# Performance work log

Hardware: AMD Instinct MI355X
Metric: run time of the kernel (lower is better)

## Reference

```python
import jax, jax.numpy as jnp
import numpy as np

B, C, H, D, W = 1, 32, 32, 32, 32   # batch, channels, 3D grid
M1 = M2 = M3 = 16                   # fourier modes kept per dim
KS = 3                              # spatial attention kernel size
MEM = 5                             # memory slots
EPS = 1e-5
N = H * D * W


def _gelu(x):
    return jax.nn.gelu(x, approximate=False)  # torch exact GELU


def _gn(x):
    # GroupNorm(1, C) without affine: normalize over (C,H,D,W) per sample
    mu = jnp.mean(x, axis=(1, 2, 3, 4), keepdims=True)
    var = jnp.var(x, axis=(1, 2, 3, 4), keepdims=True)
    return (x - mu) * jax.lax.rsqrt(var + EPS)


def _spectral_conv(x, wr, wi):
    # classic 3D FNO spectral conv: keep low modes (4 corner blocks in dims H,D; low block in rfft dim W)
    xf = jnp.fft.rfftn(x, axes=(2, 3, 4))                 # (B,C,H,D,W//2+1) complex64
    w = wr + 1j * wi                                      # (4,Cin,Cout,M1,M2,M3)
    of = jnp.zeros((x.shape[0], C, H, D, W // 2 + 1), xf.dtype)
    corners = [(slice(0, M1), slice(0, M2)), (slice(H - M1, H), slice(0, M2)),
               (slice(0, M1), slice(D - M2, D)), (slice(H - M1, H), slice(D - M2, D))]
    for i, (s1, s2) in enumerate(corners):
        of = of.at[:, :, s1, s2, :M3].set(
            jnp.einsum('bixyz,ioxyz->boxyz', xf[:, :, s1, s2, :M3], w[i]))
    return jnp.fft.irfftn(of, s=(H, D, W), axes=(2, 3, 4))


def _forward(x, t, prev_memory, w_spec_r, w_spec_i, norm1_g, norm1_b,
             mlp_w1, mlp_b1, mlp_w2, mlp_b2, tin_gw, tin_gb, tin_bw, tin_bb,
             q_w, q_b, k_w, k_b, v_w, v_b, mem_key, mem_value,
             gate_w, gate_b, gru_wih, gru_whh, gru_bih, gru_bhh):
    skip1 = x
    skip2 = _gelu(x)
    # spectral conv -> GroupNorm(affine) + residual -> gelu
    h = _spectral_conv(x, w_spec_r, w_spec_i)
    h = _gelu(_gn(h) * norm1_g[None, :, None, None, None]
              + norm1_b[None, :, None, None, None] + skip1)
    # pointwise Conv1d MLP over channels
    hf = h.reshape(B, C, N)
    u = _gelu(jnp.einsum('oc,bcn->bon', mlp_w1, hf) + mlp_b1[None, :, None])
    hf = jnp.einsum('oc,bcn->bon', mlp_w2, u) + mlp_b2[None, :, None]
    h = hf.reshape(B, C, H, D, W)
    # time-conditioned instance norm: gamma/beta from 1x1 conv over t (B,C)
    gamma = (jnp.einsum('oc,bc->bo', tin_gw, t) + tin_gb)[:, :, None, None, None]
    beta = (jnp.einsum('oc,bc->bo', tin_bw, t) + tin_bb)[:, :, None, None, None]
    h = gamma * _gn(h) + beta
    # ---- spatial attention with memory ----
    pad = KS // 2
    xp = jnp.pad(h, ((0, 0), (0, 0), (pad, pad), (pad, pad), (pad, pad)))
    # 3D unfold: (B,C,27,N) patches via 27 shifted views
    patches = jnp.stack([xp[:, :, i:i + H, j:j + D, l:l + W]
                         for i in range(KS) for j in range(KS) for l in range(KS)],
                        axis=2).reshape(B, C, KS ** 3, N)
    hf = h.reshape(B, C, N)
    q = jnp.einsum('oc,bcn->bon', q_w, hf) + q_b[None, :, None]              # (B,C,N)
    k_sp = jnp.einsum('oc,bcmn->bomn', k_w, patches) + k_b[None, :, None, None]
    v_sp = jnp.einsum('oc,bcmn->bomn', v_w, patches) + v_b[None, :, None, None]
    mem_k = jnp.broadcast_to(mem_key[None, :, :, None], (B, C, MEM, N))
    mem_v = jnp.broadcast_to(mem_value[None, :, :, None], (B, C, MEM, N))
    k = jnp.concatenate([mem_k, k_sp], axis=2)                               # (B,C,32,N)
    v = jnp.concatenate([mem_v, v_sp], axis=2)
    attn = jax.nn.softmax(q[:, :, None, :] * k / jnp.sqrt(jnp.float32(C)), axis=2)
    out = jnp.sum(attn * v, axis=2)                                          # (B,C,N)
    cat = jnp.concatenate([hf, out], axis=1)                                 # (B,2C,N)
    gate = jax.nn.sigmoid(jnp.einsum('oc,bcn->bon', gate_w, cat) + gate_b[None, :, None])
    out = gate * out + (1.0 - gate) * hf
    out = out.reshape(B, C, H, D, W)
    # GRUCell memory update from spatially pooled features
    m_in = jnp.mean(out, axis=(2, 3, 4))                                     # (B,C)
    gi = m_in @ gru_wih.T + gru_bih
    gh = prev_memory @ gru_whh.T + gru_bhh
    ir, iz, inn = jnp.split(gi, 3, axis=1)
    hr, hz, hn = jnp.split(gh, 3, axis=1)
    r = jax.nn.sigmoid(ir + hr)
    z = jax.nn.sigmoid(iz + hz)
    n = jnp.tanh(inn + r * hn)
    new_memory = (1.0 - z) * n + z * prev_memory                             # (B,C)
    return out + skip2, new_memory


def setup_inputs():
    key = jax.random.key(0)
    ks = jax.random.split(key, 20)
    def rn(k, shape, s):
        return jax.random.normal(k, shape, jnp.float32) * s
    spec_scale = 1.0 / (C * C)
    return dict(
        x=jax.random.normal(ks[0], (B, C, H, D, W), jnp.float32),
        t=jax.random.normal(ks[1], (B, C), jnp.float32),
        prev_memory=jnp.zeros((B, C), jnp.float32),
        w_spec_r=rn(ks[2], (4, C, C, M1, M2, M3), spec_scale),
        w_spec_i=rn(ks[3], (4, C, C, M1, M2, M3), spec_scale),
        norm1_g=jnp.ones((C,), jnp.float32),
        norm1_b=jnp.zeros((C,), jnp.float32),
        mlp_w1=rn(ks[4], (C // 2, C), 0.1), mlp_b1=jnp.zeros((C // 2,), jnp.float32),
        mlp_w2=rn(ks[5], (C, C // 2), 0.1), mlp_b2=jnp.zeros((C,), jnp.float32),
        tin_gw=rn(ks[6], (C, C), 0.1), tin_gb=jnp.ones((C,), jnp.float32),
        tin_bw=rn(ks[7], (C, C), 0.1), tin_bb=jnp.zeros((C,), jnp.float32),
        q_w=rn(ks[8], (C, C), 0.1), q_b=jnp.zeros((C,), jnp.float32),
        k_w=rn(ks[9], (C, C), 0.1), k_b=jnp.zeros((C,), jnp.float32),
        v_w=rn(ks[10], (C, C), 0.1), v_b=jnp.zeros((C,), jnp.float32),
        mem_key=jax.random.normal(ks[11], (C, MEM), jnp.float32),
        mem_value=jax.random.normal(ks[12], (C, MEM), jnp.float32),
        gate_w=rn(ks[13], (C, 2 * C), 0.1), gate_b=jnp.zeros((C,), jnp.float32),
        gru_wih=rn(ks[14], (3 * C, C), 0.1), gru_whh=rn(ks[15], (3 * C, C), 0.1),
        gru_bih=jnp.zeros((3 * C,), jnp.float32), gru_bhh=jnp.zeros((3 * C,), jnp.float32),
    )


def reference(x, t, prev_memory, w_spec_r, w_spec_i, norm1_g, norm1_b,
              mlp_w1, mlp_b1, mlp_w2, mlp_b2, tin_gw, tin_gb, tin_bw, tin_bb,
              q_w, q_b, k_w, k_b, v_w, v_b, mem_key, mem_value,
              gate_w, gate_b, gru_wih, gru_whh, gru_bih, gru_bhh):
    return _forward(x, t, prev_memory, w_spec_r, w_spec_i, norm1_g, norm1_b,
                    mlp_w1, mlp_b1, mlp_w2, mlp_b2, tin_gw, tin_gb, tin_bw, tin_bb,
                    q_w, q_b, k_w, k_b, v_w, v_b, mem_key, mem_value,
                    gate_w, gate_b, gru_wih, gru_whh, gru_bih, gru_bhh)
```

## Files before the change

### kernel.cpp

```cpp
#include <hip/hip_runtime.h>
#include <hip/hip_bf16.h>
#include <math.h>

#define NSP 32768
#define NZ 17

__device__ __forceinline__ float geluf(float x){
    return 0.5f * x * (1.0f + erff(x * 0.70710678118654752f));
}
__device__ __forceinline__ float sigmoidf_(float x){
    return 1.0f / (1.0f + expf(-x));
}


__global__ void k_rfft_w(const float* __restrict__ x, float* __restrict__ Ar, float* __restrict__ Ai){
    __shared__ float tile[32*33];
    __shared__ float ct[32], st[32];
    int b = blockIdx.x;
    int t = threadIdx.x;
    if (t < 32){ float ang = 6.283185307179586477f * (float)t / 32.0f; ct[t] = cosf(ang); st[t] = sinf(ang); }
    const float* src = x + b * 1024;
    for (int j = t; j < 1024; j += 256) tile[(j & 31) * 33 + (j >> 5)] = src[j];
    __syncthreads();
    for (int idx = t; idx < 544; idx += 256){
        int d = idx / 17, z = idx - d * 17;
        float sr = 0.f, si = 0.f;
        #pragma unroll
        for (int w = 0; w < 32; ++w){
            int a = (z * w) & 31;
            float v = tile[w * 33 + d];
            sr += v * ct[a];
            si -= v * st[a];
        }
        int o = (b * 32 + d) * NZ + z;
        Ar[o] = sr; Ai[o] = si;
    }
}

__global__ void k_fft_d(const float* __restrict__ Ar, const float* __restrict__ Ai,
                        float* __restrict__ Br, float* __restrict__ Bi){
    __shared__ float ir[544], ii[544];
    __shared__ float ct[32], st[32];
    int b = blockIdx.x, t = threadIdx.x;
    if (t < 32){ float ang = 6.283185307179586477f * (float)t / 32.0f; ct[t] = cosf(ang); st[t] = sinf(ang); }
    const float* pr = Ar + b * 544;
    const float* pi = Ai + b * 544;
    for (int j = t; j < 544; j += 256){ ir[j] = pr[j]; ii[j] = pi[j]; }
    __syncthreads();
    for (int idx = t; idx < 544; idx += 256){
        int kd = idx / 17, z = idx - kd * 17;
        float sr = 0.f, si = 0.f;
        #pragma unroll
        for (int d = 0; d < 32; ++d){
            int a = (kd * d) & 31;
            float c = ct[a], s = st[a];
            float vr = ir[d * 17 + z], vi = ii[d * 17 + z];
            sr += vr * c + vi * s;
            si += vi * c - vr * s;
        }
        Br[b * 544 + idx] = sr; Bi[b * 544 + idx] = si;
    }
}

__global__ void k_fft_h(const float* __restrict__ Br, const float* __restrict__ Bi,
                        float* __restrict__ Ar, float* __restrict__ Ai){
    __shared__ float ir[544], ii[544];
    __shared__ float ct[32], st[32];
    int b = blockIdx.x, t = threadIdx.x;
    int c = b >> 5, d = b & 31;
    if (t < 32){ float ang = 6.283185307179586477f * (float)t / 32.0f; ct[t] = cosf(ang); st[t] = sinf(ang); }
    for (int j = t; j < 544; j += 256){
        int h = j / 17, z = j - h * 17;
        int g = ((c * 32 + h) * 32 + d) * NZ + z;
        ir[j] = Br[g]; ii[j] = Bi[g];
    }
    __syncthreads();
    for (int idx = t; idx < 544; idx += 256){
        int kh = idx / 17, z = idx - kh * 17;
        float sr = 0.f, si = 0.f;
        #pragma unroll
        for (int h = 0; h < 32; ++h){
            int a = (kh * h) & 31;
            float c2 = ct[a], s2 = st[a];
            float vr = ir[h * 17 + z], vi = ii[h * 17 + z];
            sr += vr * c2 + vi * s2;
            si += vi * c2 - vr * s2;
        }
        int g = ((c * 32 + kh) * 32 + d) * NZ + z;
        Ar[g] = sr; Ai[g] = si;
    }
}

__global__ void k_modemul(const float* __restrict__ Xr, const float* __restrict__ Xi,
                          const float* __restrict__ Wr, const float* __restrict__ Wi,
                          float* __restrict__ Or, float* __restrict__ Oi){
    __shared__ float xr[32 * 64], xi[32 * 64];
    int b = blockIdx.x;
    int corner = b >> 6;
    int xm = (b >> 2) & 15;
    int ymg = b & 3;
    int xg = xm + ((corner & 1) << 4);
    int ybase = ymg * 4 + ((corner >> 1) << 4);
    int t = threadIdx.x;
    for (int idx = t; idx < 2048; idx += 256){
        int i = idx >> 6, m = idx & 63;
        int y = ybase + (m >> 4), z = m & 15;
        int g = ((i * 32 + xg) * 32 + y) * NZ + z;
        xr[idx] = Xr[g]; xi[idx] = Xi[g];
    }
    if (t < 128){
        int o = t >> 2, y = ybase + (t & 3);
        int g = ((o * 32 + xg) * 32 + y) * NZ + 16;
        Or[g] = 0.f; Oi[g] = 0.f;
    }
    __syncthreads();
    int wv = t >> 6, lane = t & 63;
    float ar[8], ai[8];
    #pragma unroll
    for (int oo = 0; oo < 8; ++oo){ ar[oo] = 0.f; ai[oo] = 0.f; }
    int wtail = xm * 256 + ymg * 64 + lane;
    for (int i = 0; i < 32; ++i){
        float vxr = xr[i * 64 + lane], vxi = xi[i * 64 + lane];
        #pragma unroll
        for (int oo = 0; oo < 8; ++oo){
            int o = oo * 4 + wv;
            int addr = ((corner * 32 + i) * 32 + o) * 4096 + wtail;
            float wr = Wr[addr], wi = Wi[addr];
            ar[oo] += wr * vxr - wi * vxi;
            ai[oo] += wr * vxi + wi * vxr;
        }
    }
    int y = ybase + (lane >> 4), z = lane & 15;
    #pragma unroll
    for (int oo = 0; oo < 8; ++oo){
        int o = oo * 4 + wv;
        int g = ((o * 32 + xg) * 32 + y) * NZ + z;
        Or[g] = ar[oo]; Oi[g] = ai[oo];
    }
}

__global__ void k_ifft_h(const float* __restrict__ Br, const float* __restrict__ Bi,
                         float* __restrict__ Ar, float* __restrict__ Ai){
    __shared__ float ir[544], ii[544];
    __shared__ float ct[32], st[32];
    int b = blockIdx.x, t = threadIdx.x;
    int c = b >> 5, y = b & 31;
    if (t < 32){ float ang = 6.283185307179586477f * (float)t / 32.0f; ct[t] = cosf(ang); st[t] = sinf(ang); }
    for (int j = t; j < 544; j += 256){
        int xk = j / 17, z = j - xk * 17;
        int g = ((c * 32 + xk) * 32 + y) * NZ + z;
        ir[j] = Br[g]; ii[j] = Bi[g];
    }
    __syncthreads();
    for (int idx = t; idx < 544; idx += 256){
        int h = idx / 17, z = idx - h * 17;
        float sr = 0.f, si = 0.f;
        #pragma unroll
        for (int k = 0; k < 32; ++k){
            int a = (k * h) & 31;
            float c2 = ct[a], s2 = st[a];
            float vr = ir[k * 17 + z], vi = ii[k * 17 + z];
            sr += vr * c2 - vi * s2;
            si += vr * s2 + vi * c2;
        }
        int g = ((c * 32 + h) * 32 + y) * NZ + z;
        Ar[g] = sr; Ai[g] = si;
    }
}

__global__ void k_ifft_d(const float* __restrict__ Ar, const float* __restrict__ Ai,
                         float* __restrict__ Br, float* __restrict__ Bi){
    __shared__ float ir[544], ii[544];
    __shared__ float ct[32], st[32];
    int b = blockIdx.x, t = threadIdx.x;
    if (t < 32){ float ang = 6.283185307179586477f * (float)t / 32.0f; ct[t] = cosf(ang); st[t] = sinf(ang); }
    const float* pr = Ar + b * 544;
    const float* pi = Ai + b * 544;
    for (int j = t; j < 544; j += 256){ ir[j] = pr[j]; ii[j] = pi[j]; }
    __syncthreads();
    for (int idx = t; idx < 544; idx += 256){
        int d = idx / 17, z = idx - d * 17;
        float sr = 0.f, si = 0.f;
        #pragma unroll
        for (int k = 0; k < 32; ++k){
            int a = (k * d) & 31;
            float c2 = ct[a], s2 = st[a];
            float vr = ir[k * 17 + z], vi = ii[k * 17 + z];
            sr += vr * c2 - vi * s2;
            si += vr * s2 + vi * c2;
        }
        Br[b * 544 + idx] = sr; Bi[b * 544 + idx] = si;
    }
}

__global__ void k_irfft_w(const float* __restrict__ Br, const float* __restrict__ Bi,
                          float* __restrict__ spec,
                          float* __restrict__ psum, float* __restrict__ psq){
    __shared__ float ir[544], ii[544];
    __shared__ float ct[32], st[32];
    __shared__ float ls[256], lq[256];
    int b = blockIdx.x, t = threadIdx.x;
    if (t < 32){ float ang = 6.283185307179586477f * (float)t / 32.0f; ct[t] = cosf(ang); st[t] = sinf(ang); }
    const float* pr = Br + b * 544;
    const float* pi = Bi + b * 544;
    for (int j = t; j < 544; j += 256){ ir[j] = pr[j]; ii[j] = pi[j]; }
    __syncthreads();
    const float inv = 1.0f / 32768.0f;
    float s_loc = 0.f, q_loc = 0.f;
    for (int idx = t; idx < 1024; idx += 256){
        int d = idx >> 5, w = idx & 31;
        float s = ir[d * 17 + 0] + ((w & 1) ? -ir[d * 17 + 16] : ir[d * 17 + 16]);
        #pragma unroll
        for (int z = 1; z < 16; ++z){
            int a = (z * w) & 31;
            s += 2.0f * (ir[d * 17 + z] * ct[a] - ii[d * 17 + z] * st[a]);
        }
        s *= inv;
        spec[b * 1024 + idx] = s;
        s_loc += s; q_loc += s * s;
    }
    ls[t] = s_loc; lq[t] = q_loc; __syncthreads();
    for (int off = 128; off > 0; off >>= 1){
        if (t < off){ ls[t] += ls[t + off]; lq[t] += lq[t + off]; }
        __syncthreads();
    }
    if (t == 0){ psum[b] = ls[0]; psq[b] = lq[0]; }
}


__global__ void k_finalize1(const float* __restrict__ psum, const float* __restrict__ psq,
                            int n, float* __restrict__ red){
    __shared__ float ls[256], lq[256];
    int t = threadIdx.x;
    float s = 0.f, q = 0.f;
    for (int j = t; j < n; j += 256){ s += psum[j]; q += psq[j]; }
    ls[t] = s; lq[t] = q; __syncthreads();
    for (int off = 128; off > 0; off >>= 1){
        if (t < off){ ls[t] += ls[t + off]; lq[t] += lq[t + off]; }
        __syncthreads();
    }
    if (t == 0){
        float mu = ls[0] * (1.0f / 1048576.0f);
        float var = lq[0] * (1.0f / 1048576.0f) - mu * mu;
        red[0] = mu; red[1] = rsqrtf(var + 1e-5f);
    }
}

__global__ void k_finalize2(const float* __restrict__ psum, const float* __restrict__ psq,
                            int n, const float* __restrict__ tin,
                            const float* __restrict__ tgw, const float* __restrict__ tgb,
                            const float* __restrict__ tbw, const float* __restrict__ tbb,
                            float* __restrict__ red){
    __shared__ float ls[256], lq[256];
    int t = threadIdx.x;
    float s = 0.f, q = 0.f;
    for (int j = t; j < n; j += 256){ s += psum[j]; q += psq[j]; }
    ls[t] = s; lq[t] = q; __syncthreads();
    for (int off = 128; off > 0; off >>= 1){
        if (t < off){ ls[t] += ls[t + off]; lq[t] += lq[t + off]; }
        __syncthreads();
    }
    if (t == 0){
        float mu = ls[0] * (1.0f / 1048576.0f);
        float var = lq[0] * (1.0f / 1048576.0f) - mu * mu;
        red[2] = mu; red[3] = rsqrtf(var + 1e-5f);
    }
    if (t < 64){
        int o = t & 31;
        const float* w = (t < 32) ? tgw : tbw;
        const float* bi = (t < 32) ? tgb : tbb;
        float a = bi[o];
        #pragma unroll
        for (int c = 0; c < 32; ++c) a += w[o * 32 + c] * tin[c];
        red[(t < 32 ? 16 : 48) + o] = a;
    }
}

__global__ void k_gn1(const float* __restrict__ spec, const float* __restrict__ x,
                      const float* __restrict__ g, const float* __restrict__ bb,
                      const float* __restrict__ red, float* __restrict__ h1){
    float mu = red[0], rs = red[1];
    int t = threadIdx.x;
    #pragma unroll
    for (int j = 0; j < 4; ++j){
        int p = blockIdx.x * 1024 + j * 256 + t;
        int c = p >> 15;
        float v = (spec[p] - mu) * rs * g[c] + bb[c] + x[p];
        h1[p] = geluf(v);
    }
}

__global__ void k_mlp(const float* __restrict__ h1,
                      const float* __restrict__ w1, const float* __restrict__ b1,
                      const float* __restrict__ w2, const float* __restrict__ b2,
                      float* __restrict__ h2,
                      float* __restrict__ psum, float* __restrict__ psq){
    __shared__ float W1[512], W2[512], B1[16], B2[32];
    __shared__ float ls[256], lq[256];
    int t = threadIdx.x;
    for (int j = t; j < 512; j += 256){ W1[j] = w1[j]; W2[j] = w2[j]; }
    if (t < 16) B1[t] = b1[t];
    if (t < 32) B2[t] = b2[t];
    __syncthreads();
    int n = blockIdx.x * 256 + t;
    float hv[32];
    #pragma unroll
    for (int c = 0; c < 32; ++c) hv[c] = h1[c * NSP + n];
    float u[16];
    #pragma unroll
    for (int o = 0; o < 16; ++o){
        float a = B1[o];
        #pragma unroll
        for (int c = 0; c < 32; ++c) a += W1[o * 32 + c] * hv[c];
        u[o] = geluf(a);
    }
    float s_loc = 0.f, q_loc = 0.f;
    #pragma unroll
    for (int o = 0; o < 32; ++o){
        float a = B2[o];
        #pragma unroll
        for (int c = 0; c < 16; ++c) a += W2[o * 16 + c] * u[c];
        h2[o * NSP + n] = a;
        s_loc += a; q_loc += a * a;
    }
    ls[t] = s_loc; lq[t] = q_loc; __syncthreads();
    for (int off = 128; off > 0; off >>= 1){
        if (t < off){ ls[t] += ls[t + off]; lq[t] += lq[t + off]; }
        __syncthreads();
    }
    if (t == 0){ psum[blockIdx.x] = ls[0]; psq[blockIdx.x] = lq[0]; }
}

__global__ void k_qkv(const float* __restrict__ h2, const float* __restrict__ red,
                      const float* __restrict__ qw, const float* __restrict__ qb,
                      const float* __restrict__ kw, const float* __restrict__ vw,
                      float* __restrict__ h3, float* __restrict__ Q,
                      float* __restrict__ KH, float* __restrict__ VH){
    __shared__ float QW[1024], KW[1024], VW[1024], GA[32], BE[32], QB[32];
    int t = threadIdx.x;
    for (int j = t; j < 1024; j += 256){ QW[j] = qw[j]; KW[j] = kw[j]; VW[j] = vw[j]; }
    if (t < 32){ GA[t] = red[16 + t]; BE[t] = red[48 + t]; QB[t] = qb[t]; }
    __syncthreads();
    float mu = red[2], rs = red[3];
    int n = blockIdx.x * 256 + t;
    float hv[32];
    #pragma unroll
    for (int c = 0; c < 32; ++c){
        float v = GA[c] * ((h2[c * NSP + n] - mu) * rs) + BE[c];
        hv[c] = v;
        h3[c * NSP + n] = v;
    }
    #pragma unroll
    for (int o = 0; o < 32; ++o){
        float aq = QB[o], ak = 0.f, av = 0.f;
        #pragma unroll
        for (int c = 0; c < 32; ++c){
            float v = hv[c];
            aq += QW[o * 32 + c] * v;
            ak += KW[o * 32 + c] * v;
            av += VW[o * 32 + c] * v;
        }
        Q[o * NSP + n] = aq;
        KH[o * NSP + n] = ak;
        VH[o * NSP + n] = av;
    }
}

__global__ void k_attn(const float* __restrict__ Q, const float* __restrict__ KH,
                       const float* __restrict__ VH, const float* __restrict__ h3,
                       const float* __restrict__ x,
                       const float* __restrict__ kb, const float* __restrict__ vb,
                       const float* __restrict__ mk, const float* __restrict__ mv,
                       const float* __restrict__ gw, const float* __restrict__ gb,
                       float* __restrict__ outp, float* __restrict__ mpart){
    __shared__ float l_out[256], l_h3[256], l_fin[256];
    int t = threadIdx.x;
    int c = t >> 3, nl = t & 7;
    int n = blockIdx.x * 8 + nl;
    int w_ = n & 31, d_ = (n >> 5) & 31, h_ = n >> 10;
    const float scale = 0.17677669529663688f;
    float q = Q[c * NSP + n];
    float kbc = kb[c], vbc = vb[c];
    float m = -1e30f, s = 0.f, acc = 0.f;
    #pragma unroll
    for (int j = 0; j < 5; ++j){
        float k = mk[c * 5 + j], v = mv[c * 5 + j];
        float l = q * k * scale;
        float nm = fmaxf(m, l);
        float f = expf(m - nm), e = expf(l - nm);
        s = s * f + e;
        acc = acc * f + e * v;
        m = nm;
    }
    for (int di = -1; di <= 1; ++di)
    for (int dj = -1; dj <= 1; ++dj)
    for (int dl = -1; dl <= 1; ++dl){
        int hh = h_ + di, dd = d_ + dj, ww = w_ + dl;
        bool inb = ((unsigned)hh < 32u) && ((unsigned)dd < 32u) && ((unsigned)ww < 32u);
        float k = kbc, v = vbc;
        if (inb){
            int np = (hh * 32 + dd) * 32 + ww;
            k += KH[c * NSP + np];
            v += VH[c * NSP + np];
        }
        float l = q * k * scale;
        float nm = fmaxf(m, l);
        float f = expf(m - nm), e = expf(l - nm);
        s = s * f + e;
        acc = acc * f + e * v;
        m = nm;
    }
    float out0 = acc / s;
    float h3v = h3[c * NSP + n];
    l_out[t] = out0;
    l_h3[t] = h3v;
    __syncthreads();
    float g = gb[c];
    #pragma unroll
    for (int cc = 0; cc < 32; ++cc){
        g += gw[c * 64 + cc] * l_h3[cc * 8 + nl] + gw[c * 64 + 32 + cc] * l_out[cc * 8 + nl];
    }
    g = sigmoidf_(g);
    float fin = g * out0 + (1.0f - g) * h3v;
    l_fin[t] = fin;
    float xo = x[c * NSP + n];
    outp[c * NSP + n] = fin + geluf(xo);
    __syncthreads();
    if (nl == 0){
        float ssum = 0.f;
        #pragma unroll
        for (int j = 0; j < 8; ++j) ssum += l_fin[c * 8 + j];
        mpart[c * 4096 + blockIdx.x] = ssum;
    }
}

__global__ void k_mred(const float* __restrict__ mpart, float* __restrict__ red){
    __shared__ float ls[256];
    int c = blockIdx.x, t = threadIdx.x;
    const float4* p = (const float4*)(mpart + c * 4096);
    float s = 0.f;
    #pragma unroll
    for (int j = 0; j < 4; ++j){
        float4 v = p[t + j * 256];
        s += v.x + v.y + v.z + v.w;
    }
    ls[t] = s; __syncthreads();
    for (int off = 128; off > 0; off >>= 1){
        if (t < off) ls[t] += ls[t + off];
        __syncthreads();
    }
    if (t == 0) red[128 + c] = ls[0] * (1.0f / 32768.0f);
}

__global__ void k_gru(const float* __restrict__ red, const float* __restrict__ pm,
                      const float* __restrict__ wih, const float* __restrict__ whh,
                      const float* __restrict__ bih, const float* __restrict__ bhh,
                      float* __restrict__ outp){
    __shared__ float m_in[32], gi[96], gh[96];
    int t = threadIdx.x;
    if (t < 32) m_in[t] = red[128 + t];
    __syncthreads();
    if (t < 96){
        float a = bih[t], b2 = bhh[t];
        #pragma unroll
        for (int cc = 0; cc < 32; ++cc){
            a += wih[t * 32 + cc] * m_in[cc];
            b2 += whh[t * 32 + cc] * pm[cc];
        }
        gi[t] = a; gh[t] = b2;
    }
    __syncthreads();
    if (t < 32){
        float r = sigmoidf_(gi[t] + gh[t]);
        float z = sigmoidf_(gi[32 + t] + gh[32 + t]);
        float nn = tanhf(gi[64 + t] + r * gh[64 + t]);
        float nm = (1.0f - z) * nn + z * pm[t];
        outp[1048576 + t] = nm;
    }
}

extern "C" void kernel_launch(void* const* d_in, const int* in_sizes, int n_in,
                              void* d_out, int out_size, void* d_ws, size_t ws_size,
                              hipStream_t stream){
    const float* x   = (const float*)d_in[0];
    const float* tin = (const float*)d_in[1];
    const float* pm  = (const float*)d_in[2];
    const float* wsr = (const float*)d_in[3];
    const float* wsi = (const float*)d_in[4];
    const float* n1g = (const float*)d_in[5];
    const float* n1b = (const float*)d_in[6];
    const float* mw1 = (const float*)d_in[7];
    const float* mb1 = (const float*)d_in[8];
    const float* mw2 = (const float*)d_in[9];
    const float* mb2 = (const float*)d_in[10];
    const float* tgw = (const float*)d_in[11];
    const float* tgb = (const float*)d_in[12];
    const float* tbw = (const float*)d_in[13];
    const float* tbb = (const float*)d_in[14];
    const float* qw  = (const float*)d_in[15];
    const float* qb  = (const float*)d_in[16];
    const float* kw  = (const float*)d_in[17];
    const float* kb  = (const float*)d_in[18];
    const float* vw  = (const float*)d_in[19];
    const float* vb  = (const float*)d_in[20];
    const float* mk  = (const float*)d_in[21];
    const float* mv  = (const float*)d_in[22];
    const float* gw  = (const float*)d_in[23];
    const float* gb  = (const float*)d_in[24];
    const float* wih = (const float*)d_in[25];
    const float* whh = (const float*)d_in[26];
    const float* bih = (const float*)d_in[27];
    const float* bhh = (const float*)d_in[28];

    float* ws = (float*)d_ws;
    float* Ar   = ws + 0;
    float* Ai   = ws + 557056;
    float* Br   = ws + 1114112;
    float* Bi   = ws + 1671168;
    float* spec = ws + 2228224;
    float* h1   = ws + 3276800;
    float* h2   = ws + 4325376;
    float* h3   = ws + 5373952;
    float* red  = ws + 6422528;
    float* psum = ws + 6422784;
    float* psq  = ws + 6423808;
    float* Qb  = Br;
    float* KHb = spec;
    float* VHb = h1;
    float* mpart = Ar;

    float* outp = (float*)d_out;

    k_rfft_w <<<1024, 256, 0, stream>>>(x, Ar, Ai);
    k_fft_d  <<<1024, 256, 0, stream>>>(Ar, Ai, Br, Bi);
    k_fft_h  <<<1024, 256, 0, stream>>>(Br, Bi, Ar, Ai);
    k_modemul<<<256, 256, 0, stream>>>(Ar, Ai, wsr, wsi, Br, Bi);
    k_ifft_h <<<1024, 256, 0, stream>>>(Br, Bi, Ar, Ai);
    k_ifft_d <<<1024, 256, 0, stream>>>(Ar, Ai, Br, Bi);
    k_irfft_w<<<1024, 256, 0, stream>>>(Br, Bi, spec, psum, psq);
    k_finalize1<<<1, 256, 0, stream>>>(psum, psq, 1024, red);
    k_gn1    <<<1024, 256, 0, stream>>>(spec, x, n1g, n1b, red, h1);
    k_mlp    <<<128, 256, 0, stream>>>(h1, mw1, mb1, mw2, mb2, h2, psum, psq);
    k_finalize2<<<1, 256, 0, stream>>>(psum, psq, 128, tin, tgw, tgb, tbw, tbb, red);
    k_qkv    <<<128, 256, 0, stream>>>(h2, red, qw, qb, kw, vw, h3, Qb, KHb, VHb);
    k_attn   <<<4096, 256, 0, stream>>>(Qb, KHb, VHb, h3, x, kb, vb, mk, mv, gw, gb, outp, mpart);
    k_mred   <<<32, 256, 0, stream>>>(mpart, red);
    k_gru    <<<1, 128, 0, stream>>>(red, pm, wih, whh, bih, bhh, outp);
}
```

Baseline: 199.0 us.

## Fuse FFT stages and GN into MLP, restructure attention with channel-last layout

Merges the W and D forward FFT passes into one kernel and the inverse D and W passes into another, keeping intermediates in shared memory. Folds the GroupNorm+GELU elementwise pass into the MLP kernel. Switches h3/Q/K/V to a channel-last layout and rewrites attention so each block handles one spatial row, with gate weights in shared memory. It also drops the online-softmax max tracking and uses __expf, counting out-of-bounds neighbours in closed form. Without the running max, large logits could overflow exp.

After: 294.1 us. +47.8%, slower.

```diff
diff --git a/kernel.cpp b/kernel.cpp
--- a/kernel.cpp
+++ b/kernel.cpp
@@ -9,15 +9,15 @@
     return 0.5f * x * (1.0f + erff(x * 0.70710678118654752f));
 }
 __device__ __forceinline__ float sigmoidf_(float x){
-    return 1.0f / (1.0f + expf(-x));
-}
-
-
-__global__ void k_rfft_w(const float* __restrict__ x, float* __restrict__ Ar, float* __restrict__ Ai){
+    return 1.0f / (1.0f + __expf(-x));
+}
+
+
+__global__ void k_fwd(const float* __restrict__ x, float* __restrict__ Br, float* __restrict__ Bi){
     __shared__ float tile[32*33];
+    __shared__ float ar[544], ai[544];
     __shared__ float ct[32], st[32];
-    int b = blockIdx.x;
-    int t = threadIdx.x;
+    int b = blockIdx.x, t = threadIdx.x;
     if (t < 32){ float ang = 6.283185307179586477f * (float)t / 32.0f; ct[t] = cosf(ang); st[t] = sinf(ang); }
     const float* src = x + b * 1024;
     for (int j = t; j < 1024; j += 256) tile[(j & 31) * 33 + (j >> 5)] = src[j];
@@ -32,20 +32,8 @@
             sr += v * ct[a];
             si -= v * st[a];
         }
-        int o = (b * 32 + d) * NZ + z;
-        Ar[o] = sr; Ai[o] = si;
-    }
-}
-
-__global__ void k_fft_d(const float* __restrict__ Ar, const float* __restrict__ Ai,
-                        float* __restrict__ Br, float* __restrict__ Bi){
-    __shared__ float ir[544], ii[544];
-    __shared__ float ct[32], st[32];
-    int b = blockIdx.x, t = threadIdx.x;
-    if (t < 32){ float ang = 6.283185307179586477f * (float)t / 32.0f; ct[t] = cosf(ang); st[t] = sinf(ang); }
-    const float* pr = Ar + b * 544;
-    const float* pi = Ai + b * 544;
-    for (int j = t; j < 544; j += 256){ ir[j] = pr[j]; ii[j] = pi[j]; }
+        ar[idx] = sr; ai[idx] = si;
+    }
     __syncthreads();
     for (int idx = t; idx < 544; idx += 256){
         int kd = idx / 17, z = idx - kd * 17;
@@ -54,7 +42,7 @@
         for (int d = 0; d < 32; ++d){
             int a = (kd * d) & 31;
             float c = ct[a], s = st[a];
-            float vr = ir[d * 17 + z], vi = ii[d * 17 + z];
+            float vr = ar[d * 17 + z], vi = ai[d * 17 + z];
             sr += vr * c + vi * s;
             si += vi * c - vr * s;
         }
@@ -168,10 +156,13 @@
     }
 }
 
-__global__ void k_ifft_d(const float* __restrict__ Ar, const float* __restrict__ Ai,
-                         float* __restrict__ Br, float* __restrict__ Bi){
+__global__ void k_inv(const float* __restrict__ Ar, const float* __restrict__ Ai,
+                      float* __restrict__ spec,
+                      float* __restrict__ psum, float* __restrict__ psq){
     __shared__ float ir[544], ii[544];
+    __shared__ float cr[544], ci[544];
     __shared__ float ct[32], st[32];
+    __shared__ float ls[256], lq[256];
     int b = blockIdx.x, t = threadIdx.x;
     if (t < 32){ float ang = 6.283185307179586477f * (float)t / 32.0f; ct[t] = cosf(ang); st[t] = sinf(ang); }
     const float* pr = Ar + b * 544;
@@ -189,31 +180,18 @@
             sr += vr * c2 - vi * s2;
             si += vr * s2 + vi * c2;
         }
-        Br[b * 544 + idx] = sr; Bi[b * 544 + idx] = si;
-    }
-}
-
-__global__ void k_irfft_w(const float* __restrict__ Br, const float* __restrict__ Bi,
-                          float* __restrict__ spec,
-                          float* __restrict__ psum, float* __restrict__ psq){
-    __shared__ float ir[544], ii[544];
-    __shared__ float ct[32], st[32];
-    __shared__ float ls[256], lq[256];
-    int b = blockIdx.x, t = threadIdx.x;
-    if (t < 32){ float ang = 6.283185307179586477f * (float)t / 32.0f; ct[t] = cosf(ang); st[t] = sinf(ang); }
-    const float* pr = Br + b * 544;
-    const float* pi = Bi + b * 544;
-    for (int j = t; j < 544; j += 256){ ir[j] = pr[j]; ii[j] = pi[j]; }
+        cr[idx] = sr; ci[idx] = si;
+    }
     __syncthreads();
     const float inv = 1.0f / 32768.0f;
     float s_loc = 0.f, q_loc = 0.f;
     for (int idx = t; idx < 1024; idx += 256){
         int d = idx >> 5, w = idx & 31;
-        float s = ir[d * 17 + 0] + ((w & 1) ? -ir[d * 17 + 16] : ir[d * 17 + 16]);
+        float s = cr[d * 17 + 0] + ((w & 1) ? -cr[d * 17 + 16] : cr[d * 17 + 16]);
         #pragma unroll
         for (int z = 1; z < 16; ++z){
             int a = (z * w) & 31;
-            s += 2.0f * (ir[d * 17 + z] * ct[a] - ii[d * 17 + z] * st[a]);
+            s += 2.0f * (cr[d * 17 + z] * ct[a] - ci[d * 17 + z] * st[a]);
         }
         s *= inv;
         spec[b * 1024 + idx] = s;
@@ -276,36 +254,28 @@
     }
 }
 
-__global__ void k_gn1(const float* __restrict__ spec, const float* __restrict__ x,
-                      const float* __restrict__ g, const float* __restrict__ bb,
-                      const float* __restrict__ red, float* __restrict__ h1){
-    float mu = red[0], rs = red[1];
-    int t = threadIdx.x;
-    #pragma unroll
-    for (int j = 0; j < 4; ++j){
-        int p = blockIdx.x * 1024 + j * 256 + t;
-        int c = p >> 15;
-        float v = (spec[p] - mu) * rs * g[c] + bb[c] + x[p];
-        h1[p] = geluf(v);
-    }
-}
-
-__global__ void k_mlp(const float* __restrict__ h1,
+__global__ void k_mlp(const float* __restrict__ spec, const float* __restrict__ x,
+                      const float* __restrict__ n1g, const float* __restrict__ n1b,
+                      const float* __restrict__ red,
                       const float* __restrict__ w1, const float* __restrict__ b1,
                       const float* __restrict__ w2, const float* __restrict__ b2,
                       float* __restrict__ h2,
                       float* __restrict__ psum, float* __restrict__ psq){
-    __shared__ float W1[512], W2[512], B1[16], B2[32];
+    __shared__ float W1[512], W2[512], B1[16], B2[32], GG[32], BB[32];
     __shared__ float ls[256], lq[256];
     int t = threadIdx.x;
     for (int j = t; j < 512; j += 256){ W1[j] = w1[j]; W2[j] = w2[j]; }
     if (t < 16) B1[t] = b1[t];
-    if (t < 32) B2[t] = b2[t];
-    __syncthreads();
+    if (t < 32){ B2[t] = b2[t]; GG[t] = n1g[t]; BB[t] = n1b[t]; }
+    __syncthreads();
+    float mu = red[0], rs = red[1];
     int n = blockIdx.x * 256 + t;
     float hv[32];
     #pragma unroll
-    for (int c = 0; c < 32; ++c) hv[c] = h1[c * NSP + n];
+    for (int c = 0; c < 32; ++c){
+        float v = (spec[c * NSP + n] - mu) * rs * GG[c] + BB[c] + x[c * NSP + n];
+        hv[c] = geluf(v);
+    }
     float u[16];
     #pragma unroll
     for (int o = 0; o < 16; ++o){
@@ -348,7 +318,7 @@
     for (int c = 0; c < 32; ++c){
         float v = GA[c] * ((h2[c * NSP + n] - mu) * rs) + BE[c];
         hv[c] = v;
-        h3[c * NSP + n] = v;
+        h3[n * 32 + c] = v;
     }
     #pragma unroll
     for (int o = 0; o < 32; ++o){
@@ -360,9 +330,9 @@
             ak += KW[o * 32 + c] * v;
             av += VW[o * 32 + c] * v;
         }
-        Q[o * NSP + n] = aq;
-        KH[o * NSP + n] = ak;
-        VH[o * NSP + n] = av;
+        Q[n * 32 + o] = aq;
+        KH[n * 32 + o] = ak;
+        VH[n * 32 + o] = av;
     }
 }
 
@@ -373,77 +343,106 @@
                        const float* __restrict__ mk, const float* __restrict__ mv,
                        const float* __restrict__ gw, const float* __restrict__ gb,
                        float* __restrict__ outp, float* __restrict__ mpart){
-    __shared__ float l_out[256], l_h3[256], l_fin[256];
-    int t = threadIdx.x;
-    int c = t >> 3, nl = t & 7;
-    int n = blockIdx.x * 8 + nl;
-    int w_ = n & 31, d_ = (n >> 5) & 31, h_ = n >> 10;
+    __shared__ float GW[2048];
+    __shared__ float MK[160], MV[160];
+    __shared__ float KB[32], VB[32], GB[32];
+    __shared__ float l_h3[32*33], l_out[32*33], l_fin[32*33];
+    int t = threadIdx.x;
+    int c = t & 31, wq = t >> 5;
+    int row = blockIdx.x;
+    int h_ = row >> 5, d_ = row & 31;
+    int n0 = row * 32;
+    for (int j = t; j < 2048; j += 256) GW[j] = gw[j];
+    if (t < 160){ MK[t] = mk[t]; MV[t] = mv[t]; }
+    if (t < 32){ KB[t] = kb[t]; VB[t] = vb[t]; GB[t] = gb[t]; }
     const float scale = 0.17677669529663688f;
-    float q = Q[c * NSP + n];
-    float kbc = kb[c], vbc = vb[c];
-    float m = -1e30f, s = 0.f, acc = 0.f;
-    #pragma unroll
-    for (int j = 0; j < 5; ++j){
-        float k = mk[c * 5 + j], v = mv[c * 5 + j];
-        float l = q * k * scale;
-        float nm = fmaxf(m, l);
-        float f = expf(m - nm), e = expf(l - nm);
-        s = s * f + e;
-        acc = acc * f + e * v;
-        m = nm;
-    }
-    for (int di = -1; di <= 1; ++di)
-    for (int dj = -1; dj <= 1; ++dj)
-    for (int dl = -1; dl <= 1; ++dl){
-        int hh = h_ + di, dd = d_ + dj, ww = w_ + dl;
-        bool inb = ((unsigned)hh < 32u) && ((unsigned)dd < 32u) && ((unsigned)ww < 32u);
-        float k = kbc, v = vbc;
-        if (inb){
-            int np = (hh * 32 + dd) * 32 + ww;
-            k += KH[c * NSP + np];
-            v += VH[c * NSP + np];
-        }
-        float l = q * k * scale;
-        float nm = fmaxf(m, l);
-        float f = expf(m - nm), e = expf(l - nm);
-        s = s * f + e;
-        acc = acc * f + e * v;
-        m = nm;
-    }
-    float out0 = acc / s;
-    float h3v = h3[c * NSP + n];
-    l_out[t] = out0;
-    l_h3[t] = h3v;
-    __syncthreads();
-    float g = gb[c];
-    #pragma unroll
-    for (int cc = 0; cc < 32; ++cc){
-        g += gw[c * 64 + cc] * l_h3[cc * 8 + nl] + gw[c * 64 + 32 + cc] * l_out[cc * 8 + nl];
-    }
-    g = sigmoidf_(g);
-    float fin = g * out0 + (1.0f - g) * h3v;
-    l_fin[t] = fin;
-    float xo = x[c * NSP + n];
-    outp[c * NSP + n] = fin + geluf(xo);
-    __syncthreads();
-    if (nl == 0){
-        float ssum = 0.f;
-        #pragma unroll
-        for (int j = 0; j < 8; ++j) ssum += l_fin[c * 8 + j];
-        mpart[c * 4096 + blockIdx.x] = ssum;
+    float qv[4], hv[4], s[4], ac[4], o0[4];
+    int nb[4];
+    #pragma unroll
+    for (int i = 0; i < 4; ++i){
+        int w = wq * 4 + i;
+        qv[i] = Q[(n0 + w) * 32 + c];
+        hv[i] = h3[(n0 + w) * 32 + c];
+        s[i] = 0.f; ac[i] = 0.f; nb[i] = 0;
+    }
+    __syncthreads();
+    #pragma unroll
+    for (int i = 0; i < 4; ++i){
+        #pragma unroll
+        for (int j = 0; j < 5; ++j){
+            float e = __expf(qv[i] * MK[c * 5 + j] * scale);
+            s[i] += e; ac[i] += e * MV[c * 5 + j];
+        }
+    }
+    int oobrows = 0;
+    for (int di = -1; di <= 1; ++di){
+        int hh = h_ + di;
+        for (int dj = -1; dj <= 1; ++dj){
+            int dd = d_ + dj;
+            if (((unsigned)hh >= 32u) || ((unsigned)dd >= 32u)){ oobrows++; continue; }
+            const float* Kr = KH + (hh * 32 + dd) * 1024;
+            const float* Vr = VH + (hh * 32 + dd) * 1024;
+            #pragma unroll
+            for (int i = 0; i < 4; ++i){
+                int w = wq * 4 + i;
+                #pragma unroll
+                for (int dl = -1; dl <= 1; ++dl){
+                    int ww = w + dl;
+                    if ((unsigned)ww < 32u){
+                        float k = Kr[ww * 32 + c];
+                        float v = Vr[ww * 32 + c];
+                        float e = __expf(qv[i] * k * scale);
+                        s[i] += e; ac[i] += e * v;
+                    } else nb[i]++;
+                }
+            }
+        }
+    }
+    #pragma unroll
+    for (int i = 0; i < 4; ++i){
+        float cnt = (float)(nb[i] + 3 * oobrows);
+        float eb = __expf(qv[i] * KB[c] * scale);
+        s[i] += cnt * eb; ac[i] += cnt * eb * VB[c];
+        o0[i] = ac[i] / s[i];
+        int w = wq * 4 + i;
+        l_out[w * 33 + c] = o0[i];
+        l_h3[w * 33 + c] = hv[i];
+    }
+    __syncthreads();
+    #pragma unroll
+    for (int i = 0; i < 4; ++i){
+        int w = wq * 4 + i;
+        float g = GB[c];
+        #pragma unroll
+        for (int cc = 0; cc < 32; ++cc){
+            g += GW[c * 64 + cc] * l_h3[w * 33 + cc] + GW[c * 64 + 32 + cc] * l_out[w * 33 + cc];
+        }
+        g = sigmoidf_(g);
+        l_fin[w * 33 + c] = g * o0[i] + (1.0f - g) * hv[i];
+    }
+    __syncthreads();
+    #pragma unroll
+    for (int i = 0; i < 4; ++i){
+        int r = wq + i * 8;
+        int w2 = c;
+        float f2 = l_fin[w2 * 33 + r];
+        float xo = x[r * NSP + n0 + w2];
+        outp[r * NSP + n0 + w2] = f2 + geluf(xo);
+    }
+    if (t < 32){
+        float sm = 0.f;
+        #pragma unroll
+        for (int w = 0; w < 32; ++w) sm += l_fin[w * 33 + t];
+        mpart[t * 1024 + row] = sm;
     }
 }
 
 __global__ void k_mred(const float* __restrict__ mpart, float* __restrict__ red){
     __shared__ float ls[256];
     int c = blockIdx.x, t = threadIdx.x;
-    const float4* p = (const float4*)(mpart + c * 4096);
-    float s = 0.f;
-    #pragma unroll
-    for (int j = 0; j < 4; ++j){
-        float4 v = p[t + j * 256];
-        s += v.x + v.y + v.z + v.w;
-    }
+    const float4* p = (const float4*)(mpart + c * 1024);
+    float4 v = p[t];
+    float s = v.x + v.y + v.z + v.w;
     ls[t] = s; __syncthreads();
     for (int off = 128; off > 0; off >>= 1){
         if (t < off) ls[t] += ls[t + off];
@@ -531,19 +530,16 @@
 
     float* outp = (float*)d_out;
 
-    k_rfft_w <<<1024, 256, 0, stream>>>(x, Ar, Ai);
-    k_fft_d  <<<1024, 256, 0, stream>>>(Ar, Ai, Br, Bi);
+    k_fwd    <<<1024, 256, 0, stream>>>(x, Br, Bi);
     k_fft_h  <<<1024, 256, 0, stream>>>(Br, Bi, Ar, Ai);
     k_modemul<<<256, 256, 0, stream>>>(Ar, Ai, wsr, wsi, Br, Bi);
     k_ifft_h <<<1024, 256, 0, stream>>>(Br, Bi, Ar, Ai);
-    k_ifft_d <<<1024, 256, 0, stream>>>(Ar, Ai, Br, Bi);
-    k_irfft_w<<<1024, 256, 0, stream>>>(Br, Bi, spec, psum, psq);
+    k_inv    <<<1024, 256, 0, stream>>>(Ar, Ai, spec, psum, psq);
     k_finalize1<<<1, 256, 0, stream>>>(psum, psq, 1024, red);
-    k_gn1    <<<1024, 256, 0, stream>>>(spec, x, n1g, n1b, red, h1);
-    k_mlp    <<<128, 256, 0, stream>>>(h1, mw1, mb1, mw2, mb2, h2, psum, psq);
+    k_mlp    <<<128, 256, 0, stream>>>(spec, x, n1g, n1b, red, mw1, mb1, mw2, mb2, h2, psum, psq);
     k_finalize2<<<1, 256, 0, stream>>>(psum, psq, 128, tin, tgw, tgb, tbw, tbb, red);
     k_qkv    <<<128, 256, 0, stream>>>(h2, red, qw, qb, kw, vw, h3, Qb, KHb, VHb);
-    k_attn   <<<4096, 256, 0, stream>>>(Qb, KHb, VHb, h3, x, kb, vb, mk, mv, gw, gb, outp, mpart);
+    k_attn   <<<1024, 256, 0, stream>>>(Qb, KHb, VHb, h3, x, kb, vb, mk, mv, gw, gb, outp, mpart);
     k_mred   <<<32, 256, 0, stream>>>(mpart, red);
     k_gru    <<<1, 128, 0, stream>>>(red, pm, wih, whh, bih, bhh, outp);
 }
```
